# Optimization experiments

Hardware: AMD Instinct MI355X
Metric: run time of the kernel (lower is better)

## Reference

```python
import jax, jax.numpy as jnp
import numpy as np

NUM_HEADS = 16


def rotate_half(x):
    x1 = x[..., ::2]
    x2 = x[..., 1::2]
    return jnp.concatenate((-x2, x1), axis=-1)


def rope_sin_cos(seq_len, head_dim, dtype):
    inv_freq = 1.0 / (10000.0 ** (jnp.arange(0, head_dim, 2, dtype=jnp.float32) / head_dim))
    t = jnp.arange(seq_len, dtype=jnp.float32)
    freqs = jnp.einsum('i,j->ij', t, inv_freq)          # [S, D/2]
    emb = jnp.concatenate((freqs, freqs), axis=-1)      # [S, D]
    return jnp.sin(emb).astype(dtype), jnp.cos(emb).astype(dtype)


def setup_inputs() -> dict:
    key = jax.random.key(0)
    B, S, E = 2, 2048, 2048
    ks = jax.random.split(key, 5)
    scale = 1.0 / np.sqrt(E)
    return {
        'x': jax.random.normal(ks[0], (B, S, E), dtype=jnp.float32),
        'mask': jnp.ones((B, S), dtype=jnp.int32),
        'Wq': jax.random.normal(ks[1], (E, E), dtype=jnp.float32) * scale,
        'bq': jnp.zeros((E,), dtype=jnp.float32),
        'Wk': jax.random.normal(ks[2], (E, E), dtype=jnp.float32) * scale,
        'bk': jnp.zeros((E,), dtype=jnp.float32),
        'Wv': jax.random.normal(ks[3], (E, E), dtype=jnp.float32) * scale,
        'bv': jnp.zeros((E,), dtype=jnp.float32),
        'Wo': jax.random.normal(ks[4], (E, E), dtype=jnp.float32) * scale,
        'bo': jnp.zeros((E,), dtype=jnp.float32),
    }


def reference(x, mask, Wq, bq, Wk, bk, Wv, bv, Wo, bo):
    B, S, E = x.shape
    H = NUM_HEADS
    D = E // H
    q = (x @ Wq + bq).reshape(B, S, H, D).transpose(0, 2, 1, 3)  # [B,H,S,D]
    k = (x @ Wk + bk).reshape(B, S, H, D).transpose(0, 2, 1, 3)
    v = (x @ Wv + bv).reshape(B, S, H, D).transpose(0, 2, 1, 3)

    sin, cos = rope_sin_cos(S, D, q.dtype)  # [S,D]
    sin = sin[None, None]                    # [1,1,S,D]
    cos = cos[None, None]
    q = q * cos + rotate_half(q) * sin
    k = k * cos + rotate_half(k) * sin

    scores = jnp.einsum('bhqd,bhkd->bhqk', q, k) / jnp.sqrt(jnp.asarray(D, q.dtype))
    scores = jnp.where(mask[:, None, None, :] == 0, -jnp.inf, scores)
    probs = jax.nn.softmax(scores, axis=-1)
    attn = jnp.einsum('bhqk,bhkd->bhqd', probs, v)       # [B,H,S,D]
    attn = attn.transpose(0, 2, 1, 3).reshape(B, S, E)
    return attn @ Wo + bo
```

## Files before the change

kernel.cpp:

```cpp
#include <hip/hip_runtime.h>
#include <hip/hip_bf16.h>
#include <cmath>

typedef unsigned short u16;
typedef unsigned int   u32;

using v4f = __attribute__((ext_vector_type(4))) float;
using s8v = __attribute__((ext_vector_type(8))) short;

union Frag { uint4 u; s8v s; };

__device__ __forceinline__ u16 f2bf(float f){
  u32 u = __float_as_uint(f);
  u32 r = u + 0x7fffu + ((u >> 16) & 1u);
  return (u16)(r >> 16);
}
__device__ __forceinline__ float bf2f(u16 h){ return __uint_as_float(((u32)h) << 16); }

__device__ __forceinline__ void async16(const void* g, void* l){
  __builtin_amdgcn_global_load_lds((__attribute__((address_space(1))) void*)g,
                                   (__attribute__((address_space(3))) void*)l, 16, 0, 0);
}

__global__ __launch_bounds__(256) void cast_x_kernel(const float* __restrict__ x, u16* __restrict__ xb){
  size_t i = ((size_t)blockIdx.x * 256 + threadIdx.x) * 4;
  float4 v = *(const float4*)(x + i);
  uint2 o;
  o.x = (u32)f2bf(v.x) | ((u32)f2bf(v.y) << 16);
  o.y = (u32)f2bf(v.z) | ((u32)f2bf(v.w) << 16);
  *(uint2*)(xb + i) = o;
}

__global__ __launch_bounds__(256) void cast_transpose_kernel(
    const float* __restrict__ W0, const float* __restrict__ W1,
    const float* __restrict__ W2, const float* __restrict__ W3,
    u16* __restrict__ T0, u16* __restrict__ T1, u16* __restrict__ T2, u16* __restrict__ T3){
  __shared__ float tile[64][65];
  const float* W = (blockIdx.z==0)?W0:(blockIdx.z==1)?W1:(blockIdx.z==2)?W2:W3;
  u16*         T = (blockIdx.z==0)?T0:(blockIdx.z==1)?T1:(blockIdx.z==2)?T2:T3;
  const int k0 = blockIdx.y*64, n0 = blockIdx.x*64;
  const int t  = threadIdx.x;
  const int rr = t >> 4, c4 = (t & 15) * 4;
  #pragma unroll
  for (int i=0;i<4;i++){
    int k = rr + i*16;
    float4 v = *(const float4*)(W + (size_t)(k0+k)*2048 + n0 + c4);
    tile[k][c4+0]=v.x; tile[k][c4+1]=v.y; tile[k][c4+2]=v.z; tile[k][c4+3]=v.w;
  }
  __syncthreads();
  #pragma unroll
  for (int i=0;i<4;i++){
    int n = rr + i*16;
    uint2 o;
    o.x = (u32)f2bf(tile[c4+0][n]) | ((u32)f2bf(tile[c4+1][n])<<16);
    o.y = (u32)f2bf(tile[c4+2][n]) | ((u32)f2bf(tile[c4+3][n])<<16);
    *(uint2*)(T + (size_t)(n0+n)*2048 + k0 + c4) = o;
  }
}

template<int MODE>
__global__ __launch_bounds__(256) void gemm_kernel(const u16* __restrict__ A,
                                                   const u16* __restrict__ BT,
                                                   const float* __restrict__ bias,
                                                   void* __restrict__ Cout){
  constexpr int K = 2048;
  __shared__ u16 Asl[128*64];
  __shared__ u16 Bsl[128*64];
  const int tid  = threadIdx.x;
  const int w    = tid >> 6;
  const int lane = tid & 63;
  const int r    = lane & 15, q = lane >> 4;
  const int m0   = blockIdx.y * 128;
  const int n0   = blockIdx.x * 128;
  const int wm   = (w >> 1) * 64, wn = (w & 1) * 64;

  v4f acc[4][4];
  #pragma unroll
  for (int i=0;i<4;i++)
    #pragma unroll
    for (int j=0;j<4;j++) acc[i][j] = (v4f)0.f;

  const int srow = w*32 + (lane>>3);
  const int sblk = (lane&7) ^ ((lane>>3)&7);
  const u16* Ag = A  + (size_t)(m0+srow)*K + sblk*8;
  const u16* Bg = BT + (size_t)(n0+srow)*K + sblk*8;
  u16* Als = Asl + (w*32)*64;
  u16* Bls = Bsl + (w*32)*64;

  for (int kk = 0; kk < K; kk += 64) {
    #pragma unroll
    for (int i=0;i<4;i++){
      async16(Ag + (size_t)i*8*K + kk, Als + i*512);
      async16(Bg + (size_t)i*8*K + kk, Bls + i*512);
    }
    __syncthreads();
    #pragma unroll
    for (int ks=0; ks<2; ++ks) {
      s8v af[4], bfr[4];
      #pragma unroll
      for (int i=0;i<4;i++){
        int rho = wm + i*16 + r;
        int p = (ks*4 + q) ^ (r&7);
        Frag t; t.u = *(const uint4*)(Asl + rho*64 + p*8); af[i] = t.s;
      }
      #pragma unroll
      for (int j=0;j<4;j++){
        int rho = wn + j*16 + r;
        int p = (ks*4 + q) ^ (r&7);
        Frag t; t.u = *(const uint4*)(Bsl + rho*64 + p*8); bfr[j] = t.s;
      }
      #pragma unroll
      for (int i=0;i<4;i++)
        #pragma unroll
        for (int j=0;j<4;j++)
          acc[i][j] = __builtin_amdgcn_mfma_f32_16x16x32_bf16(af[i], bfr[j], acc[i][j], 0, 0, 0);
    }
    __syncthreads();
  }

  float bv[4];
  #pragma unroll
  for (int j=0;j<4;j++) bv[j] = bias[n0 + wn + j*16 + r];

  #pragma unroll
  for (int i=0;i<4;i++){
    #pragma unroll
    for (int j=0;j<4;j++){
      const int gn = n0 + wn + j*16 + r;
      #pragma unroll
      for (int rr2=0; rr2<4; ++rr2){
        const int gm = m0 + wm + i*16 + q*4 + rr2;
        float val = acc[i][j][rr2] + bv[j];
        if (MODE == 0) ((u16*)Cout)[(size_t)gm*2048 + gn] = f2bf(val);
        else           ((float*)Cout)[(size_t)gm*2048 + gn] = val;
      }
    }
  }
}

__global__ __launch_bounds__(256) void rope_kernel(u16* __restrict__ Q, u16* __restrict__ Kb){
  const int wrow = blockIdx.x*4 + (threadIdx.x >> 6);
  const int lane = threadIdx.x & 63;
  u16* P = (blockIdx.y == 0) ? Q : Kb;
  const int s = (wrow >> 4) & 2047;
  const size_t base = (size_t)wrow * 128;
  float invf = exp2f(-(float)lane * 0.20762050593045952f);
  float angle = (float)s * invf;
  float sn, cs;
  sincosf(angle, &sn, &cs);
  float x_j   = bf2f(P[base + lane]);
  float x_j64 = bf2f(P[base + 64 + lane]);
  float x_2j  = bf2f(P[base + 2*lane]);
  float x_2j1 = bf2f(P[base + 2*lane + 1]);
  float o0 = x_j  * cs - x_2j1 * sn;
  float o1 = x_j64 * cs + x_2j  * sn;
  P[base + lane]      = f2bf(o0);
  P[base + 64 + lane] = f2bf(o1);
}

__global__ __launch_bounds__(256) void transpose_v_kernel(const u16* __restrict__ V, u16* __restrict__ VT){
  __shared__ u16 t[64*72];
  const int s0 = blockIdx.x*64;
  const int d0 = blockIdx.y*64;
  const int bh = blockIdx.z;
  const int b = bh >> 4, h = bh & 15;
  const size_t obase = ((size_t)bh*128 + d0)*2048 + s0;
  const int tid = threadIdx.x;
  #pragma unroll
  for (int i=0;i<2;i++){
    int c = tid + i*256;
    int sl = c >> 3, dc = (c & 7) * 8;
    *(uint4*)(t + sl*72 + dc) =
      *(const uint4*)(V + ((size_t)(b*2048 + s0 + sl))*2048 + h*128 + d0 + dc);
  }
  __syncthreads();
  #pragma unroll
  for (int i=0;i<2;i++){
    int c = tid + i*256;
    int dl = c >> 3, sc4 = (c & 7) * 8;
    u16 tmp[8];
    #pragma unroll
    for (int j=0;j<8;j++) tmp[j] = t[(sc4+j)*72 + dl];
    *(uint4*)(VT + obase + (size_t)dl*2048 + sc4) = *(const uint4*)tmp;
  }
}

__global__ __launch_bounds__(256,4) void attn_kernel(const u16* __restrict__ Q,
                                                     const u16* __restrict__ K,
                                                     const u16* __restrict__ VT,
                                                     const int* __restrict__ mask,
                                                     u16* __restrict__ Out){
  constexpr int S = 2048;
  constexpr float SL2 = 0.08838834764831845f * 1.4426950408889634f;
  __shared__ u16 smem[20480];
  u16* KQlds = smem;
  u16* Vlds  = smem + 8192;
  u16* Plds  = smem + 16384;

  const int tid = threadIdx.x, w = tid >> 6, lane = tid & 63;
  const int r = lane & 15, q = lane >> 4;
  const int h = blockIdx.y, b = blockIdx.z;
  const int q0 = blockIdx.x * 64;
  const size_t rowb = (size_t)b * 2048;
  const size_t bhD  = ((size_t)(b*16 + h)) * 128;

  const int sr4 = lane >> 4;
  const int sp16 = lane & 15;
  #pragma unroll
  for (int i=0;i<4;i++){
    int R = w*16 + i*4;
    int blk = sp16 ^ ((R&7) + sr4);
    async16(Q + (rowb + q0 + R + sr4)*2048 + h*128 + blk*8, KQlds + R*128);
  }
  __syncthreads();
  s8v qf[4];
  #pragma unroll
  for (int kc=0;kc<4;kc++){
    int rho = w*16 + r;
    int p = (kc*4 + q) ^ (r&7);
    Frag t; t.u = *(const uint4*)(KQlds + rho*128 + p*8);
    qf[kc] = t.s;
  }
  __syncthreads();

  v4f accO[8];
  #pragma unroll
  for (int n=0;n<8;n++) accO[n] = (v4f)0.f;
  float lsum[4] = {0.f, 0.f, 0.f, 0.f};

  u16* Pw = Plds + w*1024;

  const int vr8 = lane >> 3;
  const int vblk = (lane&7) ^ ((lane>>3)&7);

  for (int it=0; it<32; ++it){
    const int key0 = it*64;
    #pragma unroll
    for (int i=0;i<4;i++){
      int R = w*16 + i*4;
      int blk = sp16 ^ ((R&7) + sr4);
      async16(K + (rowb + key0 + R + sr4)*2048 + h*128 + blk*8, KQlds + R*128);
    }
    #pragma unroll
    for (int i=0;i<4;i++){
      int R = w*32 + i*8;
      async16(VT + (bhD + R + vr8)*2048 + key0 + vblk*8, Vlds + R*64);
    }
    __syncthreads();

    v4f sc[4];
    #pragma unroll
    for (int n=0;n<4;n++){
      v4f a = (v4f)0.f;
      #pragma unroll
      for (int kc=0;kc<4;kc++){
        int rho = n*16 + r;
        int p = (kc*4 + q) ^ (r&7);
        Frag t; t.u = *(const uint4*)(KQlds + rho*128 + p*8);
        a = __builtin_amdgcn_mfma_f32_16x16x32_bf16(qf[kc], t.s, a, 0, 0, 0);
      }
      sc[n] = a;
    }

    int mv[4];
    #pragma unroll
    for (int n=0;n<4;n++) mv[n] = mask[b*S + key0 + n*16 + r];

    #pragma unroll
    for (int g=0;g<4;g++){
      const int row = q*4 + g;
      const int rb = row*64 + (r&7);
      #pragma unroll
      for (int n=0;n<4;n++){
        float p = exp2f(sc[n][g] * SL2);
        if (mv[n] == 0) p = 0.f;
        lsum[g] += p;
        int pp = (n*2 + (r>>3)) ^ (row&7);
        Pw[rb + pp*8] = f2bf(p);
      }
    }

    #pragma unroll
    for (int kc=0;kc<2;kc++){
      int p = (kc*4 + q) ^ (r&7);
      Frag tp; tp.u = *(const uint4*)(Pw + r*64 + p*8);
      #pragma unroll
      for (int n=0;n<8;n++){
        int d = n*16 + r;
        Frag tv; tv.u = *(const uint4*)(Vlds + d*64 + p*8);
        accO[n] = __builtin_amdgcn_mfma_f32_16x16x32_bf16(tp.s, tv.s, accO[n], 0, 0, 0);
      }
    }
    __syncthreads();
  }

  float inv[4];
  #pragma unroll
  for (int g=0;g<4;g++){
    float s = lsum[g];
    #pragma unroll
    for (int off=1; off<16; off<<=1) s += __shfl_xor(s, off, 64);
    inv[g] = (s > 0.f) ? 1.f/s : 0.f;
  }

  #pragma unroll
  for (int n=0;n<8;n++){
    #pragma unroll
    for (int g=0;g<4;g++){
      int s = q0 + w*16 + q*4 + g;
      int col = h*128 + n*16 + r;
      Out[(rowb + s)*2048 + col] = f2bf(accO[n][g] * inv[g]);
    }
  }
}

extern "C" void kernel_launch(void* const* d_in, const int* in_sizes, int n_in,
                              void* d_out, int out_size, void* d_ws, size_t ws_size,
                              hipStream_t stream) {
  (void)in_sizes; (void)n_in; (void)out_size; (void)ws_size;
  const float* x    = (const float*)d_in[0];
  const int*   mask = (const int*)d_in[1];
  const float* Wq   = (const float*)d_in[2];
  const float* bq   = (const float*)d_in[3];
  const float* Wk   = (const float*)d_in[4];
  const float* bk   = (const float*)d_in[5];
  const float* Wv   = (const float*)d_in[6];
  const float* bv   = (const float*)d_in[7];
  const float* Wo   = (const float*)d_in[8];
  const float* bo   = (const float*)d_in[9];

  u16* xbf = (u16*)d_ws;
  u16* WqT = xbf + 8388608;
  u16* WkT = WqT + 4194304;
  u16* WvT = WkT + 4194304;
  u16* WoT = WvT + 4194304;
  u16* Qb  = WoT + 4194304;
  u16* Kb  = Qb + 8388608;
  u16* Vb  = Kb + 8388608;
  u16* Ab  = Vb + 8388608;
  u16* VTb = Ab + 8388608;

  cast_x_kernel<<<8192, 256, 0, stream>>>(x, xbf);
  cast_transpose_kernel<<<dim3(32,32,4), 256, 0, stream>>>(Wq, Wk, Wv, Wo, WqT, WkT, WvT, WoT);
  gemm_kernel<0><<<dim3(16,32), 256, 0, stream>>>(xbf, WqT, bq, Qb);
  gemm_kernel<0><<<dim3(16,32), 256, 0, stream>>>(xbf, WkT, bk, Kb);
  gemm_kernel<0><<<dim3(16,32), 256, 0, stream>>>(xbf, WvT, bv, Vb);
  rope_kernel<<<dim3(16384,2), 256, 0, stream>>>(Qb, Kb);
  transpose_v_kernel<<<dim3(32,2,32), 256, 0, stream>>>(Vb, VTb);
  attn_kernel<<<dim3(32,16,2), 256, 0, stream>>>(Qb, Kb, VTb, mask, Ab);
  gemm_kernel<1><<<dim3(16,32), 256, 0, stream>>>(Ab, WoT, bo, (float*)d_out);
}
```

Before: 448.1 us.

## Fuse QKV GEMMs into one launch and double query rows per attention block

The three Q/K/V projection GEMMs are merged into a single launch over a 48-column grid, relying on the contiguous WqT/WkT/WvT and Qb/Kb/Vb buffers and selecting bias and output by column range. The attention kernel now processes 128 query rows per block (32 per wave), so each K/V tile loaded into LDS serves twice as many MFMAs and half as many blocks reload K/V. Q fragments are read straight from global memory rather than staged through LDS. The cost is more registers and LDS per block (launch bounds reduced to 3) and fewer attention blocks, which may lower occupancy.

```diff
diff --git a/kernel.cpp b/kernel.cpp
--- a/kernel.cpp
+++ b/kernel.cpp
@@ -58,11 +58,92 @@
   }
 }
 
-template<int MODE>
-__global__ __launch_bounds__(256) void gemm_kernel(const u16* __restrict__ A,
-                                                   const u16* __restrict__ BT,
-                                                   const float* __restrict__ bias,
-                                                   void* __restrict__ Cout){
+__global__ __launch_bounds__(256) void gemm_qkv_kernel(const u16* __restrict__ A,
+                                                       const u16* __restrict__ BTall,
+                                                       const float* __restrict__ bq,
+                                                       const float* __restrict__ bk,
+                                                       const float* __restrict__ bv,
+                                                       u16* __restrict__ QKV){
+  constexpr int K = 2048;
+  __shared__ u16 Asl[128*64];
+  __shared__ u16 Bsl[128*64];
+  const int tid  = threadIdx.x;
+  const int w    = tid >> 6;
+  const int lane = tid & 63;
+  const int r    = lane & 15, q = lane >> 4;
+  const int m0   = blockIdx.y * 128;
+  const int n0g  = blockIdx.x * 128;
+  const int sel  = n0g >> 11;
+  const float* bias = (sel==0)? bq : (sel==1)? bk : bv;
+  u16* Cout = QKV + (size_t)sel * 8388608;
+  const int wm   = (w >> 1) * 64, wn = (w & 1) * 64;
+
+  v4f acc[4][4];
+  #pragma unroll
+  for (int i=0;i<4;i++)
+    #pragma unroll
+    for (int j=0;j<4;j++) acc[i][j] = (v4f)0.f;
+
+  const int srow = w*32 + (lane>>3);
+  const int sblk = (lane&7) ^ ((lane>>3)&7);
+  const u16* Ag = A     + (size_t)(m0+srow)*K + sblk*8;
+  const u16* Bg = BTall + (size_t)(n0g+srow)*K + sblk*8;
+  u16* Als = Asl + (w*32)*64;
+  u16* Bls = Bsl + (w*32)*64;
+
+  for (int kk = 0; kk < K; kk += 64) {
+    #pragma unroll
+    for (int i=0;i<4;i++){
+      async16(Ag + (size_t)i*8*K + kk, Als + i*512);
+      async16(Bg + (size_t)i*8*K + kk, Bls + i*512);
+    }
+    __syncthreads();
+    #pragma unroll
+    for (int ks=0; ks<2; ++ks) {
+      s8v af[4], bfr[4];
+      #pragma unroll
+      for (int i=0;i<4;i++){
+        int rho = wm + i*16 + r;
+        int p = (ks*4 + q) ^ (r&7);
+        Frag t; t.u = *(const uint4*)(Asl + rho*64 + p*8); af[i] = t.s;
+      }
+      #pragma unroll
+      for (int j=0;j<4;j++){
+        int rho = wn + j*16 + r;
+        int p = (ks*4 + q) ^ (r&7);
+        Frag t; t.u = *(const uint4*)(Bsl + rho*64 + p*8); bfr[j] = t.s;
+      }
+      #pragma unroll
+      for (int i=0;i<4;i++)
+        #pragma unroll
+        for (int j=0;j<4;j++)
+          acc[i][j] = __builtin_amdgcn_mfma_f32_16x16x32_bf16(af[i], bfr[j], acc[i][j], 0, 0, 0);
+    }
+    __syncthreads();
+  }
+
+  float bvv[4];
+  #pragma unroll
+  for (int j=0;j<4;j++) bvv[j] = bias[(n0g & 2047) + wn + j*16 + r];
+
+  #pragma unroll
+  for (int i=0;i<4;i++){
+    #pragma unroll
+    for (int j=0;j<4;j++){
+      const int gnl = (n0g & 2047) + wn + j*16 + r;
+      #pragma unroll
+      for (int rr2=0; rr2<4; ++rr2){
+        const int gm = m0 + wm + i*16 + q*4 + rr2;
+        Cout[(size_t)gm*2048 + gnl] = f2bf(acc[i][j][rr2] + bvv[j]);
+      }
+    }
+  }
+}
+
+__global__ __launch_bounds__(256) void gemm_out_kernel(const u16* __restrict__ A,
+                                                       const u16* __restrict__ BT,
+                                                       const float* __restrict__ bias,
+                                                       float* __restrict__ Cout){
   constexpr int K = 2048;
   __shared__ u16 Asl[128*64];
   __shared__ u16 Bsl[128*64];
@@ -118,9 +199,9 @@
     __syncthreads();
   }
 
-  float bv[4];
-  #pragma unroll
-  for (int j=0;j<4;j++) bv[j] = bias[n0 + wn + j*16 + r];
+  float bvv[4];
+  #pragma unroll
+  for (int j=0;j<4;j++) bvv[j] = bias[n0 + wn + j*16 + r];
 
   #pragma unroll
   for (int i=0;i<4;i++){
@@ -130,9 +211,7 @@
       #pragma unroll
       for (int rr2=0; rr2<4; ++rr2){
         const int gm = m0 + wm + i*16 + q*4 + rr2;
-        float val = acc[i][j][rr2] + bv[j];
-        if (MODE == 0) ((u16*)Cout)[(size_t)gm*2048 + gn] = f2bf(val);
-        else           ((float*)Cout)[(size_t)gm*2048 + gn] = val;
+        Cout[(size_t)gm*2048 + gn] = acc[i][j][rr2] + bvv[j];
       }
     }
   }
@@ -185,53 +264,50 @@
   }
 }
 
-__global__ __launch_bounds__(256,4) void attn_kernel(const u16* __restrict__ Q,
+__global__ __launch_bounds__(256,3) void attn_kernel(const u16* __restrict__ Q,
                                                      const u16* __restrict__ K,
                                                      const u16* __restrict__ VT,
                                                      const int* __restrict__ mask,
                                                      u16* __restrict__ Out){
   constexpr int S = 2048;
   constexpr float SL2 = 0.08838834764831845f * 1.4426950408889634f;
-  __shared__ u16 smem[20480];
-  u16* KQlds = smem;
-  u16* Vlds  = smem + 8192;
-  u16* Plds  = smem + 16384;
+  __shared__ u16 smem[24576];
+  u16* Klds = smem;
+  u16* Vlds = smem + 8192;
+  u16* Plds = smem + 16384;
 
   const int tid = threadIdx.x, w = tid >> 6, lane = tid & 63;
   const int r = lane & 15, q = lane >> 4;
   const int h = blockIdx.y, b = blockIdx.z;
-  const int q0 = blockIdx.x * 64;
+  const int q0 = blockIdx.x * 128;
   const size_t rowb = (size_t)b * 2048;
   const size_t bhD  = ((size_t)(b*16 + h)) * 128;
 
-  const int sr4 = lane >> 4;
-  const int sp16 = lane & 15;
-  #pragma unroll
-  for (int i=0;i<4;i++){
-    int R = w*16 + i*4;
-    int blk = sp16 ^ ((R&7) + sr4);
-    async16(Q + (rowb + q0 + R + sr4)*2048 + h*128 + blk*8, KQlds + R*128);
-  }
-  __syncthreads();
-  s8v qf[4];
-  #pragma unroll
-  for (int kc=0;kc<4;kc++){
-    int rho = w*16 + r;
-    int p = (kc*4 + q) ^ (r&7);
-    Frag t; t.u = *(const uint4*)(KQlds + rho*128 + p*8);
-    qf[kc] = t.s;
-  }
-  __syncthreads();
-
-  v4f accO[8];
-  #pragma unroll
-  for (int n=0;n<8;n++) accO[n] = (v4f)0.f;
-  float lsum[4] = {0.f, 0.f, 0.f, 0.f};
-
-  u16* Pw = Plds + w*1024;
-
-  const int vr8 = lane >> 3;
-  const int vblk = (lane&7) ^ ((lane>>3)&7);
+  s8v qf[2][4];
+  #pragma unroll
+  for (int m=0;m<2;m++){
+    #pragma unroll
+    for (int kc=0;kc<4;kc++){
+      Frag t; t.u = *(const uint4*)(Q + (rowb + q0 + w*32 + m*16 + r)*2048 + h*128 + kc*32 + q*8);
+      qf[m][kc] = t.s;
+    }
+  }
+
+  v4f accO[2][8];
+  #pragma unroll
+  for (int m=0;m<2;m++)
+    #pragma unroll
+    for (int n=0;n<8;n++) accO[m][n] = (v4f)0.f;
+  float lsum[2][4];
+  #pragma unroll
+  for (int m=0;m<2;m++)
+    #pragma unroll
+    for (int g=0;g<4;g++) lsum[m][g] = 0.f;
+
+  u16* Pw = Plds + w*2048;
+
+  const int sr4 = lane >> 4, sp16 = lane & 15;
+  const int vr8 = lane >> 3, vblk = (lane&7) ^ ((lane>>3)&7);
 
   for (int it=0; it<32; ++it){
     const int key0 = it*64;
@@ -239,7 +315,7 @@
     for (int i=0;i<4;i++){
       int R = w*16 + i*4;
       int blk = sp16 ^ ((R&7) + sr4);
-      async16(K + (rowb + key0 + R + sr4)*2048 + h*128 + blk*8, KQlds + R*128);
+      async16(K + (rowb + key0 + R + sr4)*2048 + h*128 + blk*8, Klds + R*128);
     }
     #pragma unroll
     for (int i=0;i<4;i++){
@@ -248,18 +324,19 @@
     }
     __syncthreads();
 
-    v4f sc[4];
+    v4f sc[2][4];
     #pragma unroll
     for (int n=0;n<4;n++){
-      v4f a = (v4f)0.f;
+      v4f a0 = (v4f)0.f, a1 = (v4f)0.f;
       #pragma unroll
       for (int kc=0;kc<4;kc++){
         int rho = n*16 + r;
         int p = (kc*4 + q) ^ (r&7);
-        Frag t; t.u = *(const uint4*)(KQlds + rho*128 + p*8);
-        a = __builtin_amdgcn_mfma_f32_16x16x32_bf16(qf[kc], t.s, a, 0, 0, 0);
-      }
-      sc[n] = a;
+        Frag t; t.u = *(const uint4*)(Klds + rho*128 + p*8);
+        a0 = __builtin_amdgcn_mfma_f32_16x16x32_bf16(qf[0][kc], t.s, a0, 0, 0, 0);
+        a1 = __builtin_amdgcn_mfma_f32_16x16x32_bf16(qf[1][kc], t.s, a1, 0, 0, 0);
+      }
+      sc[0][n] = a0; sc[1][n] = a1;
     }
 
     int mv[4];
@@ -267,49 +344,63 @@
     for (int n=0;n<4;n++) mv[n] = mask[b*S + key0 + n*16 + r];
 
     #pragma unroll
-    for (int g=0;g<4;g++){
-      const int row = q*4 + g;
-      const int rb = row*64 + (r&7);
-      #pragma unroll
-      for (int n=0;n<4;n++){
-        float p = exp2f(sc[n][g] * SL2);
-        if (mv[n] == 0) p = 0.f;
-        lsum[g] += p;
-        int pp = (n*2 + (r>>3)) ^ (row&7);
-        Pw[rb + pp*8] = f2bf(p);
+    for (int m=0;m<2;m++){
+      #pragma unroll
+      for (int g=0;g<4;g++){
+        const int row = m*16 + q*4 + g;
+        const int rb = row*64 + (r&7);
+        #pragma unroll
+        for (int n=0;n<4;n++){
+          float p = exp2f(sc[m][n][g] * SL2);
+          if (mv[n] == 0) p = 0.f;
+          lsum[m][g] += p;
+          int pp = (n*2 + (r>>3)) ^ (row&7);
+          Pw[rb + pp*8] = f2bf(p);
+        }
       }
     }
 
     #pragma unroll
     for (int kc=0;kc<2;kc++){
       int p = (kc*4 + q) ^ (r&7);
-      Frag tp; tp.u = *(const uint4*)(Pw + r*64 + p*8);
+      s8v pf[2];
+      #pragma unroll
+      for (int m=0;m<2;m++){
+        Frag t; t.u = *(const uint4*)(Pw + (m*16 + r)*64 + p*8);
+        pf[m] = t.s;
+      }
       #pragma unroll
       for (int n=0;n<8;n++){
-        int d = n*16 + r;
-        Frag tv; tv.u = *(const uint4*)(Vlds + d*64 + p*8);
-        accO[n] = __builtin_amdgcn_mfma_f32_16x16x32_bf16(tp.s, tv.s, accO[n], 0, 0, 0);
-      }
-    }
-    __syncthreads();
-  }
-
-  float inv[4];
-  #pragma unroll
-  for (int g=0;g<4;g++){
-    float s = lsum[g];
-    #pragma unroll
-    for (int off=1; off<16; off<<=1) s += __shfl_xor(s, off, 64);
-    inv[g] = (s > 0.f) ? 1.f/s : 0.f;
-  }
-
-  #pragma unroll
-  for (int n=0;n<8;n++){
+        Frag tv; tv.u = *(const uint4*)(Vlds + (n*16 + r)*64 + p*8);
+        accO[0][n] = __builtin_amdgcn_mfma_f32_16x16x32_bf16(pf[0], tv.s, accO[0][n], 0, 0, 0);
+        accO[1][n] = __builtin_amdgcn_mfma_f32_16x16x32_bf16(pf[1], tv.s, accO[1][n], 0, 0, 0);
+      }
+    }
+    __syncthreads();
+  }
+
+  float inv[2][4];
+  #pragma unroll
+  for (int m=0;m<2;m++){
     #pragma unroll
     for (int g=0;g<4;g++){
-      int s = q0 + w*16 + q*4 + g;
-      int col = h*128 + n*16 + r;
-      Out[(rowb + s)*2048 + col] = f2bf(accO[n][g] * inv[g]);
+      float s = lsum[m][g];
+      #pragma unroll
+      for (int off=1; off<16; off<<=1) s += __shfl_xor(s, off, 64);
+      inv[m][g] = (s > 0.f) ? 1.f/s : 0.f;
+    }
+  }
+
+  #pragma unroll
+  for (int m=0;m<2;m++){
+    #pragma unroll
+    for (int n=0;n<8;n++){
+      #pragma unroll
+      for (int g=0;g<4;g++){
+        int s = q0 + w*32 + m*16 + q*4 + g;
+        int col = h*128 + n*16 + r;
+        Out[(rowb + s)*2048 + col] = f2bf(accO[m][n][g] * inv[m][g]);
+      }
     }
   }
 }
@@ -342,11 +433,9 @@
 
   cast_x_kernel<<<8192, 256, 0, stream>>>(x, xbf);
   cast_transpose_kernel<<<dim3(32,32,4), 256, 0, stream>>>(Wq, Wk, Wv, Wo, WqT, WkT, WvT, WoT);
-  gemm_kernel<0><<<dim3(16,32), 256, 0, stream>>>(xbf, WqT, bq, Qb);
-  gemm_kernel<0><<<dim3(16,32), 256, 0, stream>>>(xbf, WkT, bk, Kb);
-  gemm_kernel<0><<<dim3(16,32), 256, 0, stream>>>(xbf, WvT, bv, Vb);
+  gemm_qkv_kernel<<<dim3(48,32), 256, 0, stream>>>(xbf, WqT, bq, bk, bv, Qb);
   rope_kernel<<<dim3(16384,2), 256, 0, stream>>>(Qb, Kb);
   transpose_v_kernel<<<dim3(32,2,32), 256, 0, stream>>>(Vb, VTb);
-  attn_kernel<<<dim3(32,16,2), 256, 0, stream>>>(Qb, Kb, VTb, mask, Ab);
-  gemm_kernel<1><<<dim3(16,32), 256, 0, stream>>>(Ab, WoT, bo, (float*)d_out);
-}
+  attn_kernel<<<dim3(16,16,2), 256, 0, stream>>>(Qb, Kb, VTb, mask, Ab);
+  gemm_out_kernel<<<dim3(16,32), 256, 0, stream>>>(Ab, WoT, bo, (float*)d_out);
+}
```

After: 493.9 us. 10.2% more time.
